# Kernel optimization log

Measured on AMD Instinct MI355X. Metric: run time of the kernel, lower is better.

The kernel has to match this reference:

```python
import jax, jax.numpy as jnp
import numpy as np

GRAY_LEVELS = 16
DISTANCE = 1
ANGLES = (0, 45, 90, 135)


def _glcm_entropy(img):
    """img: [H, W] float in [0,1). Returns scalar entropy of the pooled GLCM."""
    L = GRAY_LEVELS
    d = DISTANCE
    # torch does (img * (L-1)).to(uint8): truncation toward zero for non-negative inputs
    q = (img * (L - 1)).astype(jnp.int32)  # [H, W], values in [0, L-1]
    counts = jnp.zeros((L * L,), jnp.float32)
    for angle in ANGLES:  # small fixed loop over 4 angles
        if angle == 0:
            s = jnp.roll(q, d, axis=1)
        elif angle == 45:
            s = jnp.roll(q, (d, -d), axis=(0, 1))
        elif angle == 90:
            s = jnp.roll(q, d, axis=0)
        elif angle == 135:
            s = jnp.roll(q, (d, d), axis=(0, 1))
        else:
            raise ValueError('Unsupported angle.')
        # fused scatter-add histogram over joint (i, j) bins, replaces L^2 mask-sums
        idx = (q * L + s).reshape(-1)  # [H*W]
        counts = counts.at[idx].add(1.0)
    glcm = counts / counts.sum()
    return -jnp.sum(glcm * jnp.log(glcm + 1e-10))


def setup_inputs() -> dict:
    key = jax.random.key(0)
    x = jax.random.uniform(key, (8, 16, 512, 512), dtype=jnp.float32)
    return {"x": x}


def reference(x):
    B, C, H, W = x.shape
    ent = jax.vmap(_glcm_entropy)(x.reshape(B * C, H, W))  # [B*C]
    # each (b,c) slice of the output is filled with that image's scalar entropy
    return jnp.broadcast_to(ent.reshape(B, C, 1, 1), (B, C, H, W))
```

## Files before the change

### kernel.cpp

```cpp
#include <hip/hip_runtime.h>
#include <math.h>

#define IMG_H    512
#define IMG_W    512
#define IMG_HW   (IMG_H * IMG_W)
#define N_IMG    128
#define STRIPS   8
#define NBINS    256
#define FILL_PER_IMG 16

typedef float f32x4 __attribute__((ext_vector_type(4)));

__global__ __launch_bounds__(256) void glcm_hist_kernel(
    const float* __restrict__ x, unsigned int* __restrict__ partial) {

    __shared__ unsigned int lh[8][NBINS];
    const int tid   = threadIdx.x;
    const int bid   = blockIdx.x;
    const int img   = bid >> 3;
    const int strip = bid & 7;

    #pragma unroll
    for (int i = tid; i < 8 * NBINS; i += 256) ((unsigned int*)lh)[i] = 0u;
    __syncthreads();

    const float* __restrict__ base = x + (size_t)img * IMG_HW;
    unsigned int* mh = lh[tid >> 5];

    const int half = tid >> 7;
    const int jj   = (tid & 127) << 2;
    const int jm1  = (jj + IMG_W - 1) & (IMG_W - 1);
    const int jp4  = (jj + 4) & (IMG_W - 1);
    const int rowBase = strip * (IMG_H / STRIPS);

    for (int it = 0; it < (IMG_H / STRIPS) / 2; ++it) {
        const int r  = rowBase + it * 2 + half;
        const int ru = (r + IMG_H - 1) & (IMG_H - 1);

        const float4 c4 = *reinterpret_cast<const float4*>(base + (size_t)r  * IMG_W + jj);
        const float4 u4 = *reinterpret_cast<const float4*>(base + (size_t)ru * IMG_W + jj);
        const float  cm1 = base[(size_t)r  * IMG_W + jm1];
        const float  um1 = base[(size_t)ru * IMG_W + jm1];
        const float  up4 = base[(size_t)ru * IMG_W + jp4];

        int qc[5];
        int qu[6];
        qc[0] = (int)(cm1 * 15.0f);
        qc[1] = (int)(c4.x * 15.0f); qc[2] = (int)(c4.y * 15.0f);
        qc[3] = (int)(c4.z * 15.0f); qc[4] = (int)(c4.w * 15.0f);
        qu[0] = (int)(um1 * 15.0f);
        qu[1] = (int)(u4.x * 15.0f); qu[2] = (int)(u4.y * 15.0f);
        qu[3] = (int)(u4.z * 15.0f); qu[4] = (int)(u4.w * 15.0f);
        qu[5] = (int)(up4 * 15.0f);

        #pragma unroll
        for (int k = 0; k < 4; ++k) {
            const int q = qc[k + 1] << 4;
            atomicAdd(&mh[q + qc[k]],     1u);
            atomicAdd(&mh[q + qu[k + 2]], 1u);
            atomicAdd(&mh[q + qu[k + 1]], 1u);
            atomicAdd(&mh[q + qu[k]],     1u);
        }
    }

    __syncthreads();
    unsigned int total = 0;
    #pragma unroll
    for (int h = 0; h < 8; ++h) total += lh[h][tid];
    partial[(size_t)(img * STRIPS + strip) * NBINS + tid] = total;
}

__global__ __launch_bounds__(256) void glcm_entfill_kernel(
    const unsigned int* __restrict__ partial, float* __restrict__ out) {

    __shared__ float psum[4];
    __shared__ float ent_s;
    const int tid = threadIdx.x;
    const int bid = blockIdx.x;
    const int img = bid >> 4;
    const int sub = bid & 15;

    unsigned int c = 0;
    #pragma unroll
    for (int s = 0; s < STRIPS; ++s)
        c += partial[(size_t)(img * STRIPS + s) * NBINS + tid];

    const float p = (float)c * (1.0f / 1048576.0f);
    float t = p * logf(p + 1e-10f);
    #pragma unroll
    for (int off = 32; off > 0; off >>= 1) t += __shfl_down(t, off, 64);
    if ((tid & 63) == 0) psum[tid >> 6] = t;
    __syncthreads();
    if (tid == 0) ent_s = -(psum[0] + psum[1] + psum[2] + psum[3]);
    __syncthreads();

    const float e = ent_s;
    const f32x4 v = {e, e, e, e};
    f32x4* ob = reinterpret_cast<f32x4*>(out) +
                (size_t)img * (IMG_HW / 4) + (size_t)sub * (IMG_HW / 4 / FILL_PER_IMG);
    #pragma unroll
    for (int i = tid; i < IMG_HW / 4 / FILL_PER_IMG; i += 256)
        __builtin_nontemporal_store(v, ob + i);
}

extern "C" void kernel_launch(void* const* d_in, const int* in_sizes, int n_in,
                              void* d_out, int out_size, void* d_ws, size_t ws_size,
                              hipStream_t stream) {
    const float* x = (const float*)d_in[0];
    float* out = (float*)d_out;
    unsigned int* partial = (unsigned int*)d_ws;

    glcm_hist_kernel<<<N_IMG * STRIPS, 256, 0, stream>>>(x, partial);
    glcm_entfill_kernel<<<N_IMG * FILL_PER_IMG, 256, 0, stream>>>(partial, out);
}
```

Baseline: 69.71 us.

## Prefetch next row pair in registers and double strip count per image

```diff
diff --git a/kernel.cpp b/kernel.cpp
--- a/kernel.cpp
+++ b/kernel.cpp
@@ -5,20 +5,23 @@
 #define IMG_W    512
 #define IMG_HW   (IMG_H * IMG_W)
 #define N_IMG    128
-#define STRIPS   8
 #define NBINS    256
 #define FILL_PER_IMG 16
 
 typedef float f32x4 __attribute__((ext_vector_type(4)));
 
+template<int NSTRIPS>
 __global__ __launch_bounds__(256) void glcm_hist_kernel(
     const float* __restrict__ x, unsigned int* __restrict__ partial) {
+
+    constexpr int ROWS  = IMG_H / NSTRIPS;
+    constexpr int ITERS = ROWS / 2;
 
     __shared__ unsigned int lh[8][NBINS];
     const int tid   = threadIdx.x;
     const int bid   = blockIdx.x;
-    const int img   = bid >> 3;
-    const int strip = bid & 7;
+    const int img   = bid / NSTRIPS;
+    const int strip = bid % NSTRIPS;
 
     #pragma unroll
     for (int i = tid; i < 8 * NBINS; i += 256) ((unsigned int*)lh)[i] = 0u;
@@ -31,17 +34,30 @@
     const int jj   = (tid & 127) << 2;
     const int jm1  = (jj + IMG_W - 1) & (IMG_W - 1);
     const int jp4  = (jj + 4) & (IMG_W - 1);
-    const int rowBase = strip * (IMG_H / STRIPS);
+    const int rowBase = strip * ROWS;
 
-    for (int it = 0; it < (IMG_H / STRIPS) / 2; ++it) {
-        const int r  = rowBase + it * 2 + half;
+    float4 c4, u4; float cm1, um1, up4;
+    {
+        const int r  = rowBase + half;
         const int ru = (r + IMG_H - 1) & (IMG_H - 1);
+        c4  = *reinterpret_cast<const float4*>(base + (size_t)r  * IMG_W + jj);
+        u4  = *reinterpret_cast<const float4*>(base + (size_t)ru * IMG_W + jj);
+        cm1 = base[(size_t)r  * IMG_W + jm1];
+        um1 = base[(size_t)ru * IMG_W + jm1];
+        up4 = base[(size_t)ru * IMG_W + jp4];
+    }
 
-        const float4 c4 = *reinterpret_cast<const float4*>(base + (size_t)r  * IMG_W + jj);
-        const float4 u4 = *reinterpret_cast<const float4*>(base + (size_t)ru * IMG_W + jj);
-        const float  cm1 = base[(size_t)r  * IMG_W + jm1];
-        const float  um1 = base[(size_t)ru * IMG_W + jm1];
-        const float  up4 = base[(size_t)ru * IMG_W + jp4];
+    for (int it = 0; it < ITERS; ++it) {
+        float4 nc4, nu4; float ncm1, num1, nup4;
+        if (it + 1 < ITERS) {
+            const int r  = rowBase + (it + 1) * 2 + half;
+            const int ru = (r + IMG_H - 1) & (IMG_H - 1);
+            nc4  = *reinterpret_cast<const float4*>(base + (size_t)r  * IMG_W + jj);
+            nu4  = *reinterpret_cast<const float4*>(base + (size_t)ru * IMG_W + jj);
+            ncm1 = base[(size_t)r  * IMG_W + jm1];
+            num1 = base[(size_t)ru * IMG_W + jm1];
+            nup4 = base[(size_t)ru * IMG_W + jp4];
+        }
 
         int qc[5];
         int qu[6];
@@ -61,15 +77,18 @@
             atomicAdd(&mh[q + qu[k + 1]], 1u);
             atomicAdd(&mh[q + qu[k]],     1u);
         }
+
+        c4 = nc4; u4 = nu4; cm1 = ncm1; um1 = num1; up4 = nup4;
     }
 
     __syncthreads();
     unsigned int total = 0;
     #pragma unroll
     for (int h = 0; h < 8; ++h) total += lh[h][tid];
-    partial[(size_t)(img * STRIPS + strip) * NBINS + tid] = total;
+    partial[(size_t)(img * NSTRIPS + strip) * NBINS + tid] = total;
 }
 
+template<int NSTRIPS>
 __global__ __launch_bounds__(256) void glcm_entfill_kernel(
     const unsigned int* __restrict__ partial, float* __restrict__ out) {
 
@@ -82,8 +101,8 @@
 
     unsigned int c = 0;
     #pragma unroll
-    for (int s = 0; s < STRIPS; ++s)
-        c += partial[(size_t)(img * STRIPS + s) * NBINS + tid];
+    for (int s = 0; s < NSTRIPS; ++s)
+        c += partial[(size_t)(img * NSTRIPS + s) * NBINS + tid];
 
     const float p = (float)c * (1.0f / 1048576.0f);
     float t = p * logf(p + 1e-10f);
@@ -110,6 +129,11 @@
     float* out = (float*)d_out;
     unsigned int* partial = (unsigned int*)d_ws;
 
-    glcm_hist_kernel<<<N_IMG * STRIPS, 256, 0, stream>>>(x, partial);
-    glcm_entfill_kernel<<<N_IMG * FILL_PER_IMG, 256, 0, stream>>>(partial, out);
+    if (ws_size >= (size_t)N_IMG * 16 * NBINS * sizeof(unsigned int)) {
+        glcm_hist_kernel<16><<<N_IMG * 16, 256, 0, stream>>>(x, partial);
+        glcm_entfill_kernel<16><<<N_IMG * FILL_PER_IMG, 256, 0, stream>>>(partial, out);
+    } else {
+        glcm_hist_kernel<8><<<N_IMG * 8, 256, 0, stream>>>(x, partial);
+        glcm_entfill_kernel<8><<<N_IMG * FILL_PER_IMG, 256, 0, stream>>>(partial, out);
+    }
 }
```

Measured after the change: 67.96 us. 1.03x faster.
